# Kernel optimization log

Hardware: AMD Instinct MI355X
Metric: run time of the kernel (lower is better)

The kernel has to match this reference:

```python
import jax, jax.numpy as jnp
import numpy as np

H = 1024          # hidden_size
NH = 16           # num_heads
NKV = 16          # num_kv_heads
HD = 64           # head_dim
INTER = 2048      # intermediate_size
E = 8             # num_experts
TOPK = 2
EPS = 1e-6


def setup_inputs() -> dict:
    key = jax.random.key(0)
    ks = jax.random.split(key, 8)
    B, S = 4, 1024
    total_qkv = (NH + 2 * NKV) * HD
    return {
        "hidden_states": jax.random.normal(ks[0], (B, S, H), dtype=jnp.float32),
        "attention_mask": jnp.zeros((1, 1, S, S), dtype=jnp.float32),
        "input_layernorm": jnp.ones((H,), dtype=jnp.float32),
        "post_attention_layernorm": jnp.ones((H,), dtype=jnp.float32),
        "qkv_w": jax.random.normal(ks[1], (H, total_qkv), dtype=jnp.float32) * 0.02,
        "o_w": jax.random.normal(ks[2], (NH * HD, H), dtype=jnp.float32) * 0.02,
        "router_w": jax.random.normal(ks[3], (H, E), dtype=jnp.float32) * 0.02,
        "gate_up_proj": jax.random.normal(ks[4], (E, H, 2 * INTER), dtype=jnp.float32) * 0.02,
        "down_proj": jax.random.normal(ks[5], (E, INTER, H), dtype=jnp.float32) * 0.02,
    }


def _rmsnorm(x, w):
    var = jnp.mean(x * x, axis=-1, keepdims=True)
    return x * jax.lax.rsqrt(var + EPS) * w


def _attention_block(x, attention_mask, input_layernorm, qkv_w, o_w):
    B, S, _ = x.shape
    h = _rmsnorm(x, input_layernorm)
    qkv = h @ qkv_w  # [B,S,(NH+2*NKV)*HD]
    tq, tkv = NH * HD, NKV * HD
    q = qkv[..., :tq].reshape(B, S, NH, HD).transpose(0, 2, 1, 3)
    k = qkv[..., tq:tq + tkv].reshape(B, S, NKV, HD).transpose(0, 2, 1, 3)
    v = qkv[..., tq + tkv:].reshape(B, S, NKV, HD).transpose(0, 2, 1, 3)
    scores = jnp.einsum('bhqd,bhkd->bhqk', q, k) / np.sqrt(HD).astype(np.float32)
    scores = scores + attention_mask
    attn = jax.nn.softmax(scores, axis=-1)
    out = jnp.einsum('bhqk,bhkd->bhqd', attn, v)
    out = out.transpose(0, 2, 1, 3).reshape(B, S, NH * HD)
    return out @ o_w


def _moe_block(x, post_attention_layernorm, router_w, gate_up_proj, down_proj):
    B, S, _ = x.shape
    xf = x.reshape(-1, H)                      # [T,H]
    T = xf.shape[0]
    hf = _rmsnorm(xf, post_attention_layernorm)
    logits = hf @ router_w                     # [T,E]
    probs = jax.nn.softmax(logits, axis=-1)
    w, idx = jax.lax.top_k(probs, TOPK)        # [T,TOPK]
    w = w / jnp.sum(w, axis=-1, keepdims=True)
    # combine weights scattered into dense [T,E] (0 for unrouted experts)
    cw = jnp.zeros((T, E), dtype=hf.dtype).at[jnp.arange(T)[:, None], idx].add(w)
    out = jnp.zeros_like(hf)
    for e in range(E):  # fixed small expert loop, fully vectorized over tokens
        gu = hf @ gate_up_proj[e]              # [T,2*INTER]
        g, u = gu[:, :INTER], gu[:, INTER:]
        act = jax.nn.silu(g) * u
        out = out + cw[:, e:e + 1] * (act @ down_proj[e])
    return out.reshape(B, S, H)


def reference(hidden_states, attention_mask, input_layernorm, post_attention_layernorm,
              qkv_w, o_w, router_w, gate_up_proj, down_proj):
    x = hidden_states
    x = x + _attention_block(x, attention_mask, input_layernorm, qkv_w, o_w)
    x = x + _moe_block(x, post_attention_layernorm, router_w, gate_up_proj, down_proj)
    return x
```

## Files before the change

kernel.cpp:

```cpp
#include <hip/hip_runtime.h>
#include <cstdint>
#include <cmath>

#define T_TOK 4096
#define H_DIM 1024
#define QKV_N 3072
#define S_LEN 1024
#define INTER_DIM 2048
#define MAXROWS 9216

typedef unsigned short u16;
using f32x4 = __attribute__((ext_vector_type(4))) float;
using h16x8 = __attribute__((ext_vector_type(8))) _Float16;
using h16x4 = __attribute__((ext_vector_type(4))) _Float16;
using i32x4 = __attribute__((ext_vector_type(4))) int;
using u16x4 = __attribute__((ext_vector_type(4))) u16;
using u16x8 = __attribute__((ext_vector_type(8))) u16;

__device__ __forceinline__ float bf2f(u16 u){ return __uint_as_float(((uint32_t)u)<<16); }
__device__ __forceinline__ u16 f2bf(float f){
  uint32_t x = __float_as_uint(f);
  uint32_t r = x + 0x7FFFu + ((x>>16)&1u);
  return (u16)(r>>16);
}
__device__ __forceinline__ f32x4 mfma16(h16x8 a, h16x8 b, f32x4 c){
  return __builtin_amdgcn_mfma_f32_16x16x32_f16(a,b,c,0,0,0);
}
__device__ __forceinline__ float rsqrt_acc(float v){
  float r = rsqrtf(v);
  r = r*(1.5f - 0.5f*v*r*r);
  r = r*(1.5f - 0.5f*v*r*r);
  return r;
}
__device__ __forceinline__ float ldin(const void* p, size_t i, int is32){
  return is32 ? ((const float*)p)[i] : bf2f(((const u16*)p)[i]);
}
__device__ __forceinline__ int kslot_sw(int k, int noct){
  return (k&7) | (((k>>3) ^ (noct&3))<<3);
}
__device__ __forceinline__ void gll16(const void* g, void* l){
  __builtin_amdgcn_global_load_lds(
      (const __attribute__((address_space(1))) void*)g,
      (__attribute__((address_space(3))) void*)l, 16, 0, 0);
}

__global__ void k_detect(const uint32_t* __restrict__ x, int* __restrict__ dflag){
  uint32_t u = x[threadIdx.x];
  int e = (u>>23)&0xFF;
  int ok = (e>=103 && e<=150);
  unsigned long long m = __ballot(ok);
  if (threadIdx.x==0) *dflag = (__popcll(m) >= 48) ? 1 : 0;
}

__global__ __launch_bounds__(256) void k_trans2(const void* __restrict__ src,
    _Float16* __restrict__ dst, int R, int C, const int* __restrict__ df){
  const int is32 = *df;
  __shared__ _Float16 t[64][65];
  size_t bo = (size_t)blockIdx.z * R * C;
  int c0 = blockIdx.x<<6, r0 = blockIdx.y<<6;
  int ty = threadIdx.x>>3, tx = threadIdx.x&7;
  #pragma unroll
  for (int rr=0; rr<2; rr++){
    int r = rr*32 + ty;
    size_t gi = bo + (size_t)(r0+r)*C + c0 + tx*8;
    _Float16 v[8];
    if (is32){
      f32x4 a0 = *(const f32x4*)&((const float*)src)[gi];
      f32x4 a1 = *(const f32x4*)&((const float*)src)[gi+4];
      #pragma unroll
      for (int i=0;i<4;i++){ v[i]=(_Float16)a0[i]; v[4+i]=(_Float16)a1[i]; }
    } else {
      u16x8 a = *(const u16x8*)&((const u16*)src)[gi];
      #pragma unroll
      for (int i=0;i<8;i++) v[i]=(_Float16)bf2f(a[i]);
    }
    #pragma unroll
    for (int i=0;i<8;i++) t[r][tx*8+i] = v[i];
  }
  __syncthreads();
  #pragma unroll
  for (int rr=0; rr<2; rr++){
    int n = rr*32 + ty;
    h16x8 v;
    #pragma unroll
    for (int i=0;i<8;i++) v[i] = t[tx*8+i][n];
    *(h16x8*)&dst[bo + (size_t)(c0+n)*R + r0 + tx*8] = v;
  }
}

__global__ __launch_bounds__(256) void k_maskchk(const void* __restrict__ m, int* __restrict__ flag,
                                                 const int* __restrict__ df){
  const int is32 = *df;
  int i = (blockIdx.x*256 + threadIdx.x)*4;
  int nz = 0;
  if (is32){
    f32x4 v = *(const f32x4*)&((const float*)m)[i];
    nz = (v[0]!=0.f)||(v[1]!=0.f)||(v[2]!=0.f)||(v[3]!=0.f);
  } else {
    u16x4 v = *(const u16x4*)&((const u16*)m)[i];
    nz = ((v[0]|v[1]|v[2]|v[3]) & 0x7FFF) != 0;
  }
  if (nz) atomicOr(flag, 1);
}

__global__ __launch_bounds__(256) void k_rms1(const void* __restrict__ x, const void* __restrict__ w,
                                              float* __restrict__ h, const int* __restrict__ df){
  const int is32 = *df;
  int t = blockIdx.x, tid = threadIdx.x;
  size_t base = (size_t)t*H_DIM + tid*4;
  float f[4];
  #pragma unroll
  for (int m=0;m<4;m++) f[m] = ldin(x, base+m, is32);
  float ss = f[0]*f[0] + f[1]*f[1] + f[2]*f[2] + f[3]*f[3];
  #pragma unroll
  for (int off=32; off>0; off>>=1) ss += __shfl_down(ss, off, 64);
  __shared__ float red[4];
  if ((tid & 63) == 0) red[tid>>6] = ss;
  __syncthreads();
  float rstd = rsqrt_acc((red[0]+red[1]+red[2]+red[3]) * (1.0f/H_DIM) + 1e-6f);
  f32x4 o;
  #pragma unroll
  for (int m=0;m<4;m++) o[m] = f[m]*rstd*ldin(w, tid*4+m, is32);
  *(f32x4*)&h[base] = o;
}

template<int EPI>
__global__ __launch_bounds__(256) void k_gemm_splitA(const float* __restrict__ A,
    const _Float16* __restrict__ Bt, float* __restrict__ C, const void* __restrict__ res,
    int N, int K, const int* __restrict__ df){
  const int is32 = *df;
  __shared__ __align__(16) _Float16 Ahi[128*32];
  __shared__ __align__(16) _Float16 Alo[128*32];
  __shared__ __align__(16) _Float16 Bs[128*32];
  int tid = threadIdx.x, lane = tid&63, wvx = tid>>6;
  int wr = wvx>>1, wc = wvx&1, quad = lane>>4, lrow = lane&15;
  int m0 = blockIdx.y<<7, n0 = blockIdx.x<<7;
  f32x4 acc[4][4] = {};
  for (int k0=0; k0<K; k0+=32){
    #pragma unroll
    for (int it=0; it<4; it++){
      int ch = it*256 + tid;
      int r = ch>>3, g = ch&7;
      f32x4 v = *(const f32x4*)&A[(size_t)(m0+r)*K + k0 + g*4];
      h16x4 hi, lo;
      #pragma unroll
      for (int q2=0;q2<4;q2++){
        _Float16 hh = (_Float16)v[q2];
        hi[q2] = hh;
        lo[q2] = (_Float16)(v[q2] - (float)hh);
      }
      *(h16x4*)&Ahi[r*32 + g*4] = hi;
      *(h16x4*)&Alo[r*32 + g*4] = lo;
    }
    #pragma unroll
    for (int it=0; it<2; it++){
      int ch = it*256 + tid;
      gll16(&Bt[(size_t)(n0 + (ch>>2))*K + k0 + (ch&3)*8], &Bs[(size_t)(it*256 + wvx*64)*8]);
    }
    __syncthreads();
    h16x8 ah[4], al[4], bb[4];
    #pragma unroll
    for (int i=0;i<4;i++){
      ah[i] = *(const h16x8*)&Ahi[(wr*64 + i*16 + lrow)*32 + quad*8];
      al[i] = *(const h16x8*)&Alo[(wr*64 + i*16 + lrow)*32 + quad*8];
    }
    #pragma unroll
    for (int j=0;j<4;j++) bb[j] = *(const h16x8*)&Bs[(wc*64 + j*16 + lrow)*32 + quad*8];
    #pragma unroll
    for (int i=0;i<4;i++)
      #pragma unroll
      for (int j=0;j<4;j++){
        acc[i][j] = mfma16(ah[i], bb[j], acc[i][j]);
        acc[i][j] = mfma16(al[i], bb[j], acc[i][j]);
      }
    __syncthreads();
  }
  #pragma unroll
  for (int i=0;i<4;i++)
    #pragma unroll
    for (int j=0;j<4;j++){
      int col = n0 + wc*64 + j*16 + lrow;
      #pragma unroll
      for (int r=0;r<4;r++){
        int row = m0 + wr*64 + i*16 + quad*4 + r;
        size_t idx = (size_t)row*N + col;
        float v = acc[i][j][r];
        if (EPI==1) v += ldin(res, idx, is32);
        C[idx] = v;
      }
    }
}

__global__ __launch_bounds__(256) void k_attn(const float* __restrict__ qkv, const void* __restrict__ mask,
                                              const int* __restrict__ mflag, float* __restrict__ aout,
                                              const int* __restrict__ df){
  const int is32 = *df;
  __shared__ __align__(16) _Float16 Qhi[2*128*32], Qlo[2*128*32];
  __shared__ __align__(16) _Float16 Khi[2*32*32],  Klo[2*32*32];
  __shared__ __align__(16) _Float16 Vhi[64*32],    Vlo[64*32];
  __shared__ __align__(16) _Float16 Phi[128*32],   Plo[128*32];
  int qt = blockIdx.x, bh = blockIdx.y;
  int b = bh>>4, h = bh&15;
  int tid = threadIdx.x, lane = tid&63, wvx = tid>>6, quad = lane>>4, lrow = lane&15;
  size_t tok0 = (size_t)b*S_LEN;
  int q0 = qt<<7;
  #pragma unroll
  for (int it=0; it<8; it++){
    int idx = it*256 + tid;
    int r = idx>>4, g = idx&15;
    int d0 = g*4, p = g>>3;
    f32x4 v = *(const f32x4*)&qkv[(tok0 + q0 + r)*QKV_N + h*64 + d0];
    h16x4 hi, lo;
    #pragma unroll
    for (int m=0;m<4;m++){ _Float16 hh=(_Float16)v[m]; hi[m]=hh; lo[m]=(_Float16)(v[m]-(float)hh); }
    *(h16x4*)&Qhi[(p*128 + r)*32 + (d0&31)] = hi;
    *(h16x4*)&Qlo[(p*128 + r)*32 + (d0&31)] = lo;
  }
  int useMask = *mflag;
  float mrun[2][4], lrun[2][4];
  f32x4 oacc[2][4] = {};
  #pragma unroll
  for (int i=0;i<2;i++)
    #pragma unroll
    for (int r=0;r<4;r++){ mrun[i][r] = -INFINITY; lrun[i][r] = 0.f; }

  for (int kt=0; kt<32; kt++){
    int key0 = kt*32;
    __syncthreads();
    #pragma unroll
    for (int it=0; it<2; it++){
      int idx = it*256 + tid;
      int key = idx>>4, g = idx&15;
      int d0 = g*4, p = g>>3;
      f32x4 v = *(const f32x4*)&qkv[(tok0 + key0 + key)*QKV_N + 1024 + h*64 + d0];
      h16x4 hi, lo;
      #pragma unroll
      for (int m=0;m<4;m++){ _Float16 hh=(_Float16)v[m]; hi[m]=hh; lo[m]=(_Float16)(v[m]-(float)hh); }
      *(h16x4*)&Khi[(p*32 + key)*32 + (d0&31)] = hi;
      *(h16x4*)&Klo[(p*32 + key)*32 + (d0&31)] = lo;
    }
    #pragma unroll
    for (int it=0; it<2; it++){
      int idx = it*256 + tid;
      int key = idx & 31, dg = idx >> 5;
      int d0 = dg*4;
      f32x4 v = *(const f32x4*)&qkv[(tok0 + key0 + key)*QKV_N + 2048 + h*64 + d0];
      #pragma unroll
      for (int m=0;m<4;m++){
        _Float16 hh = (_Float16)v[m];
        Vhi[(d0+m)*32 + key] = hh;
        Vlo[(d0+m)*32 + key] = (_Float16)(v[m]-(float)hh);
      }
    }
    __syncthreads();
    f32x4 sacc[2][2] = {};
    #pragma unroll
    for (int p=0;p<2;p++){
      h16x8 qh[2], ql[2], kh[2], kl[2];
      #pragma unroll
      for (int i=0;i<2;i++){
        qh[i] = *(const h16x8*)&Qhi[(p*128 + wvx*32 + i*16 + lrow)*32 + quad*8];
        ql[i] = *(const h16x8*)&Qlo[(p*128 + wvx*32 + i*16 + lrow)*32 + quad*8];
      }
      #pragma unroll
      for (int j=0;j<2;j++){
        kh[j] = *(const h16x8*)&Khi[(p*32 + j*16 + lrow)*32 + quad*8];
        kl[j] = *(const h16x8*)&Klo[(p*32 + j*16 + lrow)*32 + quad*8];
      }
      #pragma unroll
      for (int i=0;i<2;i++)
        #pragma unroll
        for (int j=0;j<2;j++){
          sacc[i][j] = mfma16(qh[i], kh[j], sacc[i][j]);
          sacc[i][j] = mfma16(qh[i], kl[j], sacc[i][j]);
          sacc[i][j] = mfma16(ql[i], kh[j], sacc[i][j]);
        }
    }
    #pragma unroll
    for (int i=0;i<2;i++){
      #pragma unroll
      for (int r=0;r<4;r++){
        int qrow = q0 + wvx*32 + i*16 + quad*4 + r;
        #pragma unroll
        for (int j=0;j<2;j++){
          float s = sacc[i][j][r] * 0.125f;
          if (useMask) s += ldin(mask, (size_t)qrow*S_LEN + key0 + j*16 + lrow, is32);
          sacc[i][j][r] = s;
        }
        float mx = fmaxf(sacc[i][0][r], sacc[i][1][r]);
        #pragma unroll
        for (int mm=1; mm<=8; mm<<=1) mx = fmaxf(mx, __shfl_xor(mx, mm, 64));
        float mnew = fmaxf(mrun[i][r], mx);
        float alpha = __expf(mrun[i][r] - mnew);
        float ps = 0.f;
        #pragma unroll
        for (int j=0;j<2;j++){
          float p = __expf(sacc[i][j][r] - mnew);
          sacc[i][j][r] = p;
          ps += p;
        }
        #pragma unroll
        for (int mm=1; mm<=8; mm<<=1) ps += __shfl_xor(ps, mm, 64);
        lrun[i][r] = lrun[i][r]*alpha + ps;
        mrun[i][r] = mnew;
        #pragma unroll
        for (int j=0;j<4;j++) oacc[i][j][r] *= alpha;
        int prow = wvx*32 + i*16 + quad*4 + r;
        #pragma unroll
        for (int j=0;j<2;j++){
          int key = j*16 + lrow;
          float pv = sacc[i][j][r];
          _Float16 ph = (_Float16)pv;
          Phi[prow*32 + key] = ph;
          Plo[prow*32 + key] = (_Float16)(pv - (float)ph);
        }
      }
    }
    __syncthreads();
    {
      h16x8 pf[2], pl[2], vh[4], vl[4];
      #pragma unroll
      for (int i=0;i<2;i++){
        pf[i] = *(const h16x8*)&Phi[(wvx*32 + i*16 + lrow)*32 + quad*8];
        pl[i] = *(const h16x8*)&Plo[(wvx*32 + i*16 + lrow)*32 + quad*8];
      }
      #pragma unroll
      for (int j=0;j<4;j++){
        vh[j] = *(const h16x8*)&Vhi[(j*16 + lrow)*32 + quad*8];
        vl[j] = *(const h16x8*)&Vlo[(j*16 + lrow)*32 + quad*8];
      }
      #pragma unroll
      for (int i=0;i<2;i++)
        #pragma unroll
        for (int j=0;j<4;j++){
          oacc[i][j] = mfma16(pf[i], vh[j], oacc[i][j]);
          oacc[i][j] = mfma16(pf[i], vl[j], oacc[i][j]);
          oacc[i][j] = mfma16(pl[i], vh[j], oacc[i][j]);
        }
    }
  }
  #pragma unroll
  for (int i=0;i<2;i++)
    #pragma unroll
    for (int j=0;j<4;j++)
      #pragma unroll
      for (int r=0;r<4;r++){
        int row = q0 + wvx*32 + i*16 + quad*4 + r;
        int col = h*64 + j*16 + lrow;
        aout[(tok0 + row)*H_DIM + col] = oacc[i][j][r] / lrun[i][r];
      }
}

__global__ __launch_bounds__(256) void k_rms2_router(const float* __restrict__ x1, const void* __restrict__ w,
    const void* __restrict__ rw, _Float16* __restrict__ h2,
    int* __restrict__ tok_e, float* __restrict__ tok_w, int* __restrict__ counts,
    const int* __restrict__ df){
  const int is32 = *df;
  int t = blockIdx.x, tid = threadIdx.x;
  f32x4 v = *(const f32x4*)&x1[(size_t)t*H_DIM + tid*4];
  float ss = v[0]*v[0]+v[1]*v[1]+v[2]*v[2]+v[3]*v[3];
  #pragma unroll
  for (int off=32; off>0; off>>=1) ss += __shfl_down(ss, off, 64);
  __shared__ float red[4];
  __shared__ float lgs[32];
  if ((tid&63)==0) red[tid>>6] = ss;
  __syncthreads();
  float rstd = rsqrt_acc((red[0]+red[1]+red[2]+red[3])*(1.0f/H_DIM) + 1e-6f);
  float hv[4];
  h16x4 hst;
  #pragma unroll
  for (int m=0;m<4;m++){ hv[m] = v[m]*rstd*ldin(w, tid*4+m, is32); hst[m] = (_Float16)hv[m]; }
  *(h16x4*)&h2[(size_t)t*H_DIM + tid*4] = hst;
  float part[8] = {0,0,0,0,0,0,0,0};
  #pragma unroll
  for (int m=0;m<4;m++){
    size_t c = (size_t)(tid*4 + m)*8;
    #pragma unroll
    for (int e=0;e<8;e++) part[e] += hv[m]*ldin(rw, c+e, is32);
  }
  #pragma unroll
  for (int e=0;e<8;e++){
    #pragma unroll
    for (int off=32; off>0; off>>=1) part[e] += __shfl_down(part[e], off, 64);
  }
  if ((tid&63)==0){
    #pragma unroll
    for (int e=0;e<8;e++) lgs[(tid>>6)*8 + e] = part[e];
  }
  __syncthreads();
  if (tid==0){
    float lg[8];
    #pragma unroll
    for (int e=0;e<8;e++) lg[e] = lgs[e] + lgs[8+e] + lgs[16+e] + lgs[24+e];
    int e0 = 0;
    #pragma unroll
    for (int e=1;e<8;e++) if (lg[e] > lg[e0]) e0 = e;
    int e1 = (e0==0) ? 1 : 0;
    #pragma unroll
    for (int e=0;e<8;e++) if (e != e0 && lg[e] > lg[e1]) e1 = e;
    float d = expf(lg[e1] - lg[e0]);
    float w0 = 1.0f/(1.0f + d);
    float w1 = d * w0;
    tok_e[t*2] = e0; tok_e[t*2+1] = e1;
    tok_w[t*2] = w0; tok_w[t*2+1] = w1;
    atomicAdd(&counts[e0], 1);
    atomicAdd(&counts[e1], 1);
  }
}

__global__ void k_offsets(const int* __restrict__ counts, int* __restrict__ offs, int* __restrict__ fillpos){
  if (threadIdx.x == 0 && blockIdx.x == 0){
    int o = 0;
    for (int e=0;e<8;e++){
      offs[e] = o; fillpos[e] = o;
      o += (counts[e] + 127) & ~127;
    }
    offs[8] = o;
  }
}

__global__ __launch_bounds__(256) void k_fill(const int* __restrict__ tok_e, const float* __restrict__ tok_w,
    int* __restrict__ fillpos, int* __restrict__ list_ts, float* __restrict__ list_w){
  int t = blockIdx.x*256 + threadIdx.x;
  if (t >= T_TOK) return;
  #pragma unroll
  for (int s=0;s<2;s++){
    int e = tok_e[t*2+s];
    int p = atomicAdd(&fillpos[e], 1);
    list_ts[p] = t*2 + s;
    list_w[p] = tok_w[t*2+s];
  }
}


__global__ __launch_bounds__(256) void k_gemm_gu_t(const _Float16* __restrict__ h2,
    const _Float16* __restrict__ gwt, _Float16* __restrict__ act, const int* __restrict__ list_ts,
    const int* __restrict__ counts, const int* __restrict__ offs){
  int m0 = blockIdx.y<<7;
  if (m0 >= offs[8]) return;
  int e = 0;
  while (m0 >= offs[e+1]) e++;
  int base = offs[e], cnt = counts[e];
  if (m0 >= base + cnt) return;
  __shared__ __align__(16) _Float16 As[128*32], Bg[64*32], Bu[64*32];
  __shared__ int rowtok[128];
  int tid = threadIdx.x;
  if (tid < 128) rowtok[tid] = list_ts[min(m0 + tid, base + cnt - 1)] >> 1;
  __syncthreads();
  int lane = tid&63, wvx = tid>>6, wr = wvx>>1, wc = wvx&1, quad = lane>>4, lrow = lane&15;
  int n0 = blockIdx.x<<6;
  const _Float16* Bge = gwt + (size_t)e*4096*1024 + (size_t)n0*1024;
  const _Float16* Bue = gwt + (size_t)e*4096*1024 + (size_t)(2048+n0)*1024;
  const _Float16* arow0 = &h2[(size_t)rowtok[tid>>2]*H_DIM + (tid&3)*8];
  const _Float16* arow1 = &h2[(size_t)rowtok[(256+tid)>>2]*H_DIM + (tid&3)*8];
  int bR = tid>>2, bG = tid&3;
  f32x4 ag[4][2] = {}, au[4][2] = {};
  for (int k0=0; k0<1024; k0+=32){
    gll16(arow0 + k0, &As[(size_t)(wvx*64)*8]);
    gll16(arow1 + k0, &As[(size_t)(256 + wvx*64)*8]);
    gll16(&Bge[(size_t)bR*1024 + k0 + bG*8], &Bg[(size_t)(wvx*64)*8]);
    gll16(&Bue[(size_t)bR*1024 + k0 + bG*8], &Bu[(size_t)(wvx*64)*8]);
    __syncthreads();
    h16x8 a[4], bg[2], bu[2];
    #pragma unroll
    for (int i=0;i<4;i++) a[i] = *(const h16x8*)&As[(wr*64 + i*16 + lrow)*32 + quad*8];
    #pragma unroll
    for (int j=0;j<2;j++){
      bg[j] = *(const h16x8*)&Bg[(wc*32 + j*16 + lrow)*32 + quad*8];
      bu[j] = *(const h16x8*)&Bu[(wc*32 + j*16 + lrow)*32 + quad*8];
    }
    #pragma unroll
    for (int i=0;i<4;i++)
      #pragma unroll
      for (int j=0;j<2;j++){
        ag[i][j] = mfma16(a[i], bg[j], ag[i][j]);
        au[i][j] = mfma16(a[i], bu[j], au[i][j]);
      }
    __syncthreads();
  }
  #pragma unroll
  for (int i=0;i<4;i++)
    #pragma unroll
    for (int j=0;j<2;j++)
      #pragma unroll
      for (int r=0;r<4;r++){
        int row = m0 + wr*64 + i*16 + quad*4 + r;
        int col = n0 + wc*32 + j*16 + lrow;
        float g = ag[i][j][r], u = au[i][j][r];
        float sv = g / (1.0f + __expf(-g));
        act[(size_t)row*INTER_DIM + col] = (_Float16)(sv * u);
      }
}

__global__ __launch_bounds__(256) void k_gemm_down_t(const _Float16* __restrict__ act,
    const _Float16* __restrict__ dwt, _Float16* __restrict__ slotbuf, const int* __restrict__ list_ts,
    const float* __restrict__ list_w, const int* __restrict__ counts, const int* __restrict__ offs){
  int m0 = blockIdx.y<<7;
  if (m0 >= offs[8]) return;
  int e = 0;
  while (m0 >= offs[e+1]) e++;
  int base = offs[e], cnt = counts[e];
  if (m0 >= base + cnt) return;
  __shared__ __align__(16) _Float16 As[128*32], Bs[128*32];
  int tid = threadIdx.x, lane = tid&63, wvx = tid>>6;
  int wr = wvx>>1, wc = wvx&1, quad = lane>>4, lrow = lane&15;
  int n0 = blockIdx.x<<7;
  const _Float16* Be = dwt + (size_t)e*1024*2048 + (size_t)n0*2048;
  f32x4 acc[4][4] = {};
  for (int k0=0; k0<2048; k0+=32){
    #pragma unroll
    for (int it=0; it<2; it++){
      int c2 = it*256 + tid;
      int r = c2>>2, g = c2&3;
      gll16(&act[(size_t)(m0+r)*INTER_DIM + k0 + g*8], &As[(size_t)(it*256 + wvx*64)*8]);
      gll16(&Be[(size_t)r*2048 + k0 + g*8], &Bs[(size_t)(it*256 + wvx*64)*8]);
    }
    __syncthreads();
    h16x8 a[4], b[4];
    #pragma unroll
    for (int i=0;i<4;i++) a[i] = *(const h16x8*)&As[(wr*64 + i*16 + lrow)*32 + quad*8];
    #pragma unroll
    for (int j=0;j<4;j++) b[j] = *(const h16x8*)&Bs[(wc*64 + j*16 + lrow)*32 + quad*8];
    #pragma unroll
    for (int i=0;i<4;i++)
      #pragma unroll
      for (int j=0;j<4;j++)
        acc[i][j] = mfma16(a[i], b[j], acc[i][j]);
    __syncthreads();
  }
  #pragma unroll
  for (int i=0;i<4;i++)
    #pragma unroll
    for (int r=0;r<4;r++){
      int m = m0 + wr*64 + i*16 + quad*4 + r;
      if (m < base + cnt){
        int ts = list_ts[m];
        float wgt = list_w[m];
        #pragma unroll
        for (int j=0;j<4;j++){
          int col = n0 + wc*64 + j*16 + lrow;
          slotbuf[(size_t)ts*H_DIM + col] = (_Float16)(wgt * acc[i][j][r]);
        }
      }
    }
}


__global__ __launch_bounds__(256) void k_gemm_gu(const _Float16* __restrict__ h2, const void* __restrict__ guw,
    _Float16* __restrict__ act, const int* __restrict__ list_ts,
    const int* __restrict__ counts, const int* __restrict__ offs, const int* __restrict__ df){
  const int is32 = *df;
  int m0 = blockIdx.y<<7;
  if (m0 >= offs[8]) return;
  int e = 0;
  while (m0 >= offs[e+1]) e++;
  int base = offs[e], cnt = counts[e];
  if (m0 >= base + cnt) return;
  __shared__ __align__(16) _Float16 As[128*32], Bg[64*40], Bu[64*40];
  __shared__ int rowtok[128];
  int tid = threadIdx.x;
  if (tid < 128){
    int mc = min(m0 + tid, base + cnt - 1);
    rowtok[tid] = list_ts[mc] >> 1;
  }
  __syncthreads();
  int lane = tid&63, wvx = tid>>6, wr = wvx>>1, wc = wvx&1, quad = lane>>4, lrow = lane&15;
  int n0 = blockIdx.x<<6;
  size_t ebase = (size_t)e*H_DIM*4096;
  f32x4 ag[4][2] = {}, au[4][2] = {};
  for (int k0=0; k0<1024; k0+=32){
    #pragma unroll
    for (int it=0; it<2; it++){
      int ch = it*256 + tid;
      int r = ch>>2, c = ch&3;
      *(i32x4*)&As[ch*8] = *(const i32x4*)&h2[(size_t)rowtok[r]*H_DIM + k0 + c*8];
    }
    {
      int k = tid>>3, g = tid&7;
      size_t rowb = ebase + (size_t)(k0+k)*4096;
      int ks = kslot_sw(k, g);
      _Float16 tg[8], tu[8];
      if (is32){
        const float* gf = (const float*)guw;
        f32x4 a0 = *(const f32x4*)&gf[rowb + n0 + g*8];
        f32x4 a1 = *(const f32x4*)&gf[rowb + n0 + g*8 + 4];
        f32x4 b0 = *(const f32x4*)&gf[rowb + 2048 + n0 + g*8];
        f32x4 b1 = *(const f32x4*)&gf[rowb + 2048 + n0 + g*8 + 4];
        #pragma unroll
        for (int i=0;i<4;i++){ tg[i]=(_Float16)a0[i]; tg[4+i]=(_Float16)a1[i];
                               tu[i]=(_Float16)b0[i]; tu[4+i]=(_Float16)b1[i]; }
      } else {
        const u16* gb = (const u16*)guw;
        u16x4 a0 = *(const u16x4*)&gb[rowb + n0 + g*8];
        u16x4 a1 = *(const u16x4*)&gb[rowb + n0 + g*8 + 4];
        u16x4 b0 = *(const u16x4*)&gb[rowb + 2048 + n0 + g*8];
        u16x4 b1 = *(const u16x4*)&gb[rowb + 2048 + n0 + g*8 + 4];
        #pragma unroll
        for (int i=0;i<4;i++){ tg[i]=(_Float16)bf2f(a0[i]); tg[4+i]=(_Float16)bf2f(a1[i]);
                               tu[i]=(_Float16)bf2f(b0[i]); tu[4+i]=(_Float16)bf2f(b1[i]); }
      }
      #pragma unroll
      for (int i=0;i<8;i++){
        int n = g*8 + i;
        Bg[n*40 + ks] = tg[i];
        Bu[n*40 + ks] = tu[i];
      }
    }
    __syncthreads();
    h16x8 a[4], bg[2], bu[2];
    #pragma unroll
    for (int i=0;i<4;i++) a[i] = *(const h16x8*)&As[(wr*64 + i*16 + lrow)*32 + quad*8];
    #pragma unroll
    for (int j=0;j<2;j++){
      int n = wc*32 + j*16 + lrow;
      int oct = (quad ^ ((n>>3)&3))*8;
      bg[j] = *(const h16x8*)&Bg[n*40 + oct];
      bu[j] = *(const h16x8*)&Bu[n*40 + oct];
    }
    #pragma unroll
    for (int i=0;i<4;i++)
      #pragma unroll
      for (int j=0;j<2;j++){
        ag[i][j] = mfma16(a[i], bg[j], ag[i][j]);
        au[i][j] = mfma16(a[i], bu[j], au[i][j]);
      }
    __syncthreads();
  }
  #pragma unroll
  for (int i=0;i<4;i++)
    #pragma unroll
    for (int j=0;j<2;j++)
      #pragma unroll
      for (int r=0;r<4;r++){
        int row = m0 + wr*64 + i*16 + quad*4 + r;
        int col = n0 + wc*32 + j*16 + lrow;
        float g = ag[i][j][r], u = au[i][j][r];
        float sv = g / (1.0f + __expf(-g));
        act[(size_t)row*INTER_DIM + col] = (_Float16)(sv * u);
      }
}

__global__ __launch_bounds__(256) void k_gemm_down(const _Float16* __restrict__ act, const void* __restrict__ dw,
    _Float16* __restrict__ slotbuf, const int* __restrict__ list_ts, const float* __restrict__ list_w,
    const int* __restrict__ counts, const int* __restrict__ offs, const int* __restrict__ df){
  const int is32 = *df;
  int m0 = blockIdx.y<<7;
  if (m0 >= offs[8]) return;
  int e = 0;
  while (m0 >= offs[e+1]) e++;
  int base = offs[e], cnt = counts[e];
  if (m0 >= base + cnt) return;
  __shared__ __align__(16) _Float16 As[128*32], Bs[128*40];
  int tid = threadIdx.x, lane = tid&63, wvx = tid>>6;
  int wr = wvx>>1, wc = wvx&1, quad = lane>>4, lrow = lane&15;
  int n0 = blockIdx.x<<7;
  size_t ebase = (size_t)e*INTER_DIM*H_DIM;
  f32x4 acc[4][4] = {};
  for (int k0=0; k0<2048; k0+=32){
    #pragma unroll
    for (int it=0; it<2; it++){
      int ch = it*256 + tid;
      int r = ch>>2, c = ch&3;
      *(i32x4*)&As[ch*8] = *(const i32x4*)&act[(size_t)(m0+r)*INTER_DIM + k0 + c*8];
    }
    {
      int k = tid>>3, g = tid&7;
      size_t rowb = ebase + (size_t)(k0+k)*H_DIM;
      int ks = kslot_sw(k, g);
      #pragma unroll
      for (int p=0;p<2;p++){
        _Float16 tb[8];
        if (is32){
          const float* bf = (const float*)dw;
          f32x4 a0 = *(const f32x4*)&bf[rowb + n0 + p*64 + g*8];
          f32x4 a1 = *(const f32x4*)&bf[rowb + n0 + p*64 + g*8 + 4];
          #pragma unroll
          for (int i=0;i<4;i++){ tb[i]=(_Float16)a0[i]; tb[4+i]=(_Float16)a1[i]; }
        } else {
          const u16* bb = (const u16*)dw;
          u16x4 a0 = *(const u16x4*)&bb[rowb + n0 + p*64 + g*8];
          u16x4 a1 = *(const u16x4*)&bb[rowb + n0 + p*64 + g*8 + 4];
          #pragma unroll
          for (int i=0;i<4;i++){ tb[i]=(_Float16)bf2f(a0[i]); tb[4+i]=(_Float16)bf2f(a1[i]); }
        }
        #pragma unroll
        for (int i=0;i<8;i++){
          int n = p*64 + g*8 + i;
          Bs[n*40 + ks] = tb[i];
        }
      }
    }
    __syncthreads();
    h16x8 a[4], b[4];
    #pragma unroll
    for (int i=0;i<4;i++) a[i] = *(const h16x8*)&As[(wr*64 + i*16 + lrow)*32 + quad*8];
    #pragma unroll
    for (int j=0;j<4;j++){
      int n = wc*64 + j*16 + lrow;
      b[j] = *(const h16x8*)&Bs[n*40 + ((quad ^ ((n>>3)&3))*8)];
    }
    #pragma unroll
    for (int i=0;i<4;i++)
      #pragma unroll
      for (int j=0;j<4;j++)
        acc[i][j] = mfma16(a[i], b[j], acc[i][j]);
    __syncthreads();
  }
  #pragma unroll
  for (int i=0;i<4;i++)
    #pragma unroll
    for (int r=0;r<4;r++){
      int m = m0 + wr*64 + i*16 + quad*4 + r;
      if (m < base + cnt){
        int ts = list_ts[m];
        float wgt = list_w[m];
        #pragma unroll
        for (int j=0;j<4;j++){
          int col = n0 + wc*64 + j*16 + lrow;
          slotbuf[(size_t)ts*H_DIM + col] = (_Float16)(wgt * acc[i][j][r]);
        }
      }
    }
}

__global__ __launch_bounds__(256) void k_final(const float* __restrict__ x1, const _Float16* __restrict__ slot,
                                               void* __restrict__ outv, const int* __restrict__ df){
  const int is32 = *df;
  int i4 = (blockIdx.x*256 + threadIdx.x)*4;
  int t = i4 >> 10, c = i4 & 1023;
  f32x4 a = *(const f32x4*)&x1[i4];
  h16x4 s0 = *(const h16x4*)&slot[(size_t)(t*2)*H_DIM + c];
  h16x4 s1 = *(const h16x4*)&slot[(size_t)(t*2+1)*H_DIM + c];
  if (is32){
    f32x4 o;
    #pragma unroll
    for (int m=0;m<4;m++) o[m] = a[m] + (float)s0[m] + (float)s1[m];
    *(f32x4*)&((float*)outv)[i4] = o;
  } else {
    u16x4 o;
    #pragma unroll
    for (int m=0;m<4;m++) o[m] = f2bf(a[m] + (float)s0[m] + (float)s1[m]);
    *(u16x4*)&((u16*)outv)[i4] = o;
  }
}

extern "C" void kernel_launch(void* const* d_in, const int* in_sizes, int n_in,
                              void* d_out, int out_size, void* d_ws, size_t ws_size,
                              hipStream_t stream){
  (void)in_sizes; (void)n_in; (void)out_size;
  const void* x    = d_in[0];
  const void* mask = d_in[1];
  const void* ln1  = d_in[2];
  const void* ln2  = d_in[3];
  const void* qkvw = d_in[4];
  const void* ow   = d_in[5];
  const void* rw   = d_in[6];
  const void* guw  = d_in[7];
  const void* dww  = d_in[8];

  char* ws = (char*)d_ws;
  size_t off = 0;
  auto alloc = [&](size_t b)->void*{ void* p = ws + off; off = (off + b + 255) & ~(size_t)255; return p; };
  int* meta            = (int*)alloc(32*sizeof(int));
  _Float16* qkv_wt     = (_Float16*)alloc((size_t)3072*1024*2);
  _Float16* o_wt       = (_Float16*)alloc((size_t)1024*1024*2);
  float* hbuf          = (float*)alloc((size_t)4096*1024*4);
  float* qkvbuf        = (float*)alloc((size_t)4096*3072*4);
  float* x1            = (float*)alloc((size_t)4096*1024*4);
  int* list_ts         = (int*)alloc(MAXROWS*4);
  float* list_w        = (float*)alloc(MAXROWS*4);
  int* tok_e           = (int*)alloc((size_t)4096*2*4);
  float* tok_w         = (float*)alloc((size_t)4096*2*4);
  size_t base_end = off;
  _Float16* gu_wt      = (_Float16*)alloc((size_t)8*4096*1024*2);
  _Float16* down_wt    = (_Float16*)alloc((size_t)8*1024*2048*2);
  const int big = (ws_size >= off) ? 1 : 0;
  (void)base_end;

  int* counts = meta;
  int* offs   = meta + 8;
  int* fillpos= meta + 17;
  int* flag   = meta + 25;
  int* dflag  = meta + 26;
  _Float16* h2      = (_Float16*)qkvbuf;
  _Float16* act     = (_Float16*)((char*)qkvbuf + (size_t)4096*1024*2);
  _Float16* slotbuf = (_Float16*)hbuf;

  hipMemsetAsync(meta, 0, 32*sizeof(int), stream);
  k_detect<<<dim3(1), dim3(64), 0, stream>>>((const uint32_t*)x, dflag);
  k_trans2<<<dim3(48, 16, 1), 256, 0, stream>>>(qkvw, qkv_wt, 1024, 3072, dflag);
  k_trans2<<<dim3(16, 16, 1), 256, 0, stream>>>(ow, o_wt, 1024, 1024, dflag);
  if (big){
    k_trans2<<<dim3(64, 16, 8), 256, 0, stream>>>(guw, gu_wt, 1024, 4096, dflag);
    k_trans2<<<dim3(16, 32, 8), 256, 0, stream>>>(dww, down_wt, 2048, 1024, dflag);
  }
  k_maskchk<<<dim3(1024), 256, 0, stream>>>(mask, flag, dflag);
  k_rms1<<<dim3(4096), 256, 0, stream>>>(x, ln1, hbuf, dflag);
  k_gemm_splitA<0><<<dim3(24, 32), 256, 0, stream>>>(hbuf, qkv_wt, qkvbuf, nullptr, 3072, 1024, dflag);
  k_attn<<<dim3(8, 64), 256, 0, stream>>>(qkvbuf, mask, flag, hbuf, dflag);
  k_gemm_splitA<1><<<dim3(8, 32), 256, 0, stream>>>(hbuf, o_wt, x1, x, 1024, 1024, dflag);
  k_rms2_router<<<dim3(4096), 256, 0, stream>>>(x1, ln2, rw, h2, tok_e, tok_w, counts, dflag);
  k_offsets<<<dim3(1), dim3(64), 0, stream>>>(counts, offs, fillpos);
  k_fill<<<dim3(16), 256, 0, stream>>>(tok_e, tok_w, fillpos, list_ts, list_w);
  if (big){
    k_gemm_gu_t<<<dim3(32, 72), 256, 0, stream>>>(h2, gu_wt, act, list_ts, counts, offs);
    k_gemm_down_t<<<dim3(8, 72), 256, 0, stream>>>(act, down_wt, slotbuf, list_ts, list_w, counts, offs);
  } else {
    k_gemm_gu<<<dim3(32, 72), 256, 0, stream>>>(h2, guw, act, list_ts, counts, offs, dflag);
    k_gemm_down<<<dim3(8, 72), 256, 0, stream>>>(act, dww, slotbuf, list_ts, list_w, counts, offs, dflag);
  }
  k_final<<<dim3(4096), 256, 0, stream>>>(x1, slotbuf, d_out, dflag);
}
```

Baseline: 920.0 us.

## Store activations as pre-split fp16 hi/lo pairs and pre-transpose V for attention

RMSNorm, the QKV GEMM and attention now emit fp16 hi/lo split pairs instead of fp32, so the downstream GEMMs and attention load their operands directly into LDS with async global-to-LDS copies and skip the per-tile split and convert work. A new kernel pre-transposes V into a per-head dim-major layout so attention can load V tiles without scattered LDS stores. Attention also keeps Q fragments in registers, shares one LDS pool, raises wave priority around the MFMA blocks and sets launch bounds to 3 blocks. This costs an extra kernel launch and repurposes buffers (x1 holds the transposed V), which adds aliasing risk.

```diff
diff --git a/kernel.cpp b/kernel.cpp
--- a/kernel.cpp
+++ b/kernel.cpp
@@ -104,7 +104,8 @@
 }
 
 __global__ __launch_bounds__(256) void k_rms1(const void* __restrict__ x, const void* __restrict__ w,
-                                              float* __restrict__ h, const int* __restrict__ df){
+                                              _Float16* __restrict__ hhi, _Float16* __restrict__ hlo,
+                                              const int* __restrict__ df){
   const int is32 = *df;
   int t = blockIdx.x, tid = threadIdx.x;
   size_t base = (size_t)t*H_DIM + tid*4;
@@ -118,51 +119,51 @@
   if ((tid & 63) == 0) red[tid>>6] = ss;
   __syncthreads();
   float rstd = rsqrt_acc((red[0]+red[1]+red[2]+red[3]) * (1.0f/H_DIM) + 1e-6f);
-  f32x4 o;
-  #pragma unroll
-  for (int m=0;m<4;m++) o[m] = f[m]*rstd*ldin(w, tid*4+m, is32);
-  *(f32x4*)&h[base] = o;
+  h16x4 oh, ol;
+  #pragma unroll
+  for (int m=0;m<4;m++){
+    float v = f[m]*rstd*ldin(w, tid*4+m, is32);
+    _Float16 hh = (_Float16)v;
+    oh[m] = hh;
+    ol[m] = (_Float16)(v - (float)hh);
+  }
+  *(h16x4*)&hhi[base] = oh;
+  *(h16x4*)&hlo[base] = ol;
 }
 
 template<int EPI>
-__global__ __launch_bounds__(256) void k_gemm_splitA(const float* __restrict__ A,
-    const _Float16* __restrict__ Bt, float* __restrict__ C, const void* __restrict__ res,
-    int N, int K, const int* __restrict__ df){
-  const int is32 = *df;
-  __shared__ __align__(16) _Float16 Ahi[128*32];
-  __shared__ __align__(16) _Float16 Alo[128*32];
+__global__ __launch_bounds__(256) void k_gemm_hl(const _Float16* __restrict__ Ah,
+    const _Float16* __restrict__ Al, const _Float16* __restrict__ Bt,
+    float* __restrict__ C, _Float16* __restrict__ Chi, _Float16* __restrict__ Clo,
+    const void* __restrict__ res, int N, int K, const int* __restrict__ df){
+  const int is32 = (EPI==1) ? *df : 0;
+  __shared__ __align__(16) _Float16 AhS[128*32];
+  __shared__ __align__(16) _Float16 AlS[128*32];
   __shared__ __align__(16) _Float16 Bs[128*32];
   int tid = threadIdx.x, lane = tid&63, wvx = tid>>6;
   int wr = wvx>>1, wc = wvx&1, quad = lane>>4, lrow = lane&15;
   int m0 = blockIdx.y<<7, n0 = blockIdx.x<<7;
+  int ar = tid>>2, acg = (tid&3)*8;
+  const _Float16* a0h = &Ah[(size_t)(m0+ar)*K + acg];
+  const _Float16* a1h = &Ah[(size_t)(m0+64+ar)*K + acg];
+  const _Float16* a0l = &Al[(size_t)(m0+ar)*K + acg];
+  const _Float16* a1l = &Al[(size_t)(m0+64+ar)*K + acg];
+  const _Float16* b0  = &Bt[(size_t)(n0+ar)*K + acg];
+  const _Float16* b1  = &Bt[(size_t)(n0+64+ar)*K + acg];
   f32x4 acc[4][4] = {};
   for (int k0=0; k0<K; k0+=32){
-    #pragma unroll
-    for (int it=0; it<4; it++){
-      int ch = it*256 + tid;
-      int r = ch>>3, g = ch&7;
-      f32x4 v = *(const f32x4*)&A[(size_t)(m0+r)*K + k0 + g*4];
-      h16x4 hi, lo;
-      #pragma unroll
-      for (int q2=0;q2<4;q2++){
-        _Float16 hh = (_Float16)v[q2];
-        hi[q2] = hh;
-        lo[q2] = (_Float16)(v[q2] - (float)hh);
-      }
-      *(h16x4*)&Ahi[r*32 + g*4] = hi;
-      *(h16x4*)&Alo[r*32 + g*4] = lo;
-    }
-    #pragma unroll
-    for (int it=0; it<2; it++){
-      int ch = it*256 + tid;
-      gll16(&Bt[(size_t)(n0 + (ch>>2))*K + k0 + (ch&3)*8], &Bs[(size_t)(it*256 + wvx*64)*8]);
-    }
+    gll16(a0h + k0, &AhS[wvx*512]);
+    gll16(a1h + k0, &AhS[2048 + wvx*512]);
+    gll16(a0l + k0, &AlS[wvx*512]);
+    gll16(a1l + k0, &AlS[2048 + wvx*512]);
+    gll16(b0  + k0, &Bs[wvx*512]);
+    gll16(b1  + k0, &Bs[2048 + wvx*512]);
     __syncthreads();
     h16x8 ah[4], al[4], bb[4];
     #pragma unroll
     for (int i=0;i<4;i++){
-      ah[i] = *(const h16x8*)&Ahi[(wr*64 + i*16 + lrow)*32 + quad*8];
-      al[i] = *(const h16x8*)&Alo[(wr*64 + i*16 + lrow)*32 + quad*8];
+      ah[i] = *(const h16x8*)&AhS[(wr*64 + i*16 + lrow)*32 + quad*8];
+      al[i] = *(const h16x8*)&AlS[(wr*64 + i*16 + lrow)*32 + quad*8];
     }
     #pragma unroll
     for (int j=0;j<4;j++) bb[j] = *(const h16x8*)&Bs[(wc*64 + j*16 + lrow)*32 + quad*8];
@@ -185,37 +186,87 @@
         int row = m0 + wr*64 + i*16 + quad*4 + r;
         size_t idx = (size_t)row*N + col;
         float v = acc[i][j][r];
-        if (EPI==1) v += ldin(res, idx, is32);
-        C[idx] = v;
-      }
-    }
-}
-
-__global__ __launch_bounds__(256) void k_attn(const float* __restrict__ qkv, const void* __restrict__ mask,
-                                              const int* __restrict__ mflag, float* __restrict__ aout,
-                                              const int* __restrict__ df){
+        if (EPI==1){
+          v += ldin(res, idx, is32);
+          C[idx] = v;
+        } else {
+          _Float16 hh = (_Float16)v;
+          Chi[idx] = hh;
+          Clo[idx] = (_Float16)(v - (float)hh);
+        }
+      }
+    }
+}
+
+__global__ __launch_bounds__(256) void k_vt(const _Float16* __restrict__ qh,
+    const _Float16* __restrict__ ql, _Float16* __restrict__ vth, _Float16* __restrict__ vtl){
+  __shared__ _Float16 th[64][72];
+  __shared__ _Float16 tl[64][72];
+  int bh = blockIdx.y;
+  int b = bh>>4, h = bh&15;
+  int key0 = blockIdx.x<<6;
+  size_t tok0 = (size_t)b*S_LEN;
+  int ty = threadIdx.x>>3, tx = threadIdx.x&7;
+  #pragma unroll
+  for (int rr=0; rr<2; rr++){
+    int r = rr*32 + ty;
+    size_t gi = (tok0 + key0 + r)*(size_t)QKV_N + 2048 + h*64 + tx*8;
+    h16x8 vh_ = *(const h16x8*)&qh[gi];
+    h16x8 vl_ = *(const h16x8*)&ql[gi];
+    #pragma unroll
+    for (int i=0;i<8;i++){ th[r][tx*8+i] = vh_[i]; tl[r][tx*8+i] = vl_[i]; }
+  }
+  __syncthreads();
+  size_t dbase = (size_t)bh*64*1024;
+  #pragma unroll
+  for (int rr=0; rr<2; rr++){
+    int d = rr*32 + ty;
+    h16x8 oh, ol;
+    #pragma unroll
+    for (int i=0;i<8;i++){ oh[i] = th[tx*8+i][d]; ol[i] = tl[tx*8+i][d]; }
+    *(h16x8*)&vth[dbase + (size_t)d*1024 + key0 + tx*8] = oh;
+    *(h16x8*)&vtl[dbase + (size_t)d*1024 + key0 + tx*8] = ol;
+  }
+}
+
+__global__ __launch_bounds__(256, 3) void k_attn(const _Float16* __restrict__ qkvh,
+    const _Float16* __restrict__ qkvl, const _Float16* __restrict__ vth_g,
+    const _Float16* __restrict__ vtl_g, const void* __restrict__ mask,
+    const int* __restrict__ mflag, _Float16* __restrict__ ohi, _Float16* __restrict__ olo,
+    const int* __restrict__ df){
   const int is32 = *df;
-  __shared__ __align__(16) _Float16 Qhi[2*128*32], Qlo[2*128*32];
-  __shared__ __align__(16) _Float16 Khi[2*32*32],  Klo[2*32*32];
-  __shared__ __align__(16) _Float16 Vhi[64*32],    Vlo[64*32];
-  __shared__ __align__(16) _Float16 Phi[128*32],   Plo[128*32];
+  __shared__ __align__(16) _Float16 pool[16384];
   int qt = blockIdx.x, bh = blockIdx.y;
   int b = bh>>4, h = bh&15;
   int tid = threadIdx.x, lane = tid&63, wvx = tid>>6, quad = lane>>4, lrow = lane&15;
   size_t tok0 = (size_t)b*S_LEN;
   int q0 = qt<<7;
-  #pragma unroll
-  for (int it=0; it<8; it++){
-    int idx = it*256 + tid;
-    int r = idx>>4, g = idx&15;
-    int d0 = g*4, p = g>>3;
-    f32x4 v = *(const f32x4*)&qkv[(tok0 + q0 + r)*QKV_N + h*64 + d0];
-    h16x4 hi, lo;
-    #pragma unroll
-    for (int m=0;m<4;m++){ _Float16 hh=(_Float16)v[m]; hi[m]=hh; lo[m]=(_Float16)(v[m]-(float)hh); }
-    *(h16x4*)&Qhi[(p*128 + r)*32 + (d0&31)] = hi;
-    *(h16x4*)&Qlo[(p*128 + r)*32 + (d0&31)] = lo;
-  }
+  {
+    int r = tid>>2, cg = (tid&3)*8;
+    #pragma unroll
+    for (int p=0;p<2;p++)
+      #pragma unroll
+      for (int g=0;g<2;g++){
+        size_t src = (tok0 + q0 + g*64 + r)*(size_t)QKV_N + h*64 + p*32 + cg;
+        gll16(&qkvh[src], &pool[p*4096 + g*2048 + wvx*512]);
+        gll16(&qkvl[src], &pool[8192 + p*4096 + g*2048 + wvx*512]);
+      }
+  }
+  __syncthreads();
+  h16x8 qfh[2][2], qfl[2][2];
+  #pragma unroll
+  for (int p=0;p<2;p++)
+    #pragma unroll
+    for (int i=0;i<2;i++){
+      qfh[p][i] = *(const h16x8*)&pool[(p*128 + wvx*32 + i*16 + lrow)*32 + quad*8];
+      qfl[p][i] = *(const h16x8*)&pool[8192 + (p*128 + wvx*32 + i*16 + lrow)*32 + quad*8];
+    }
+  _Float16* Khi = pool;
+  _Float16* Klo = pool + 2048;
+  _Float16* Vth = pool + 4096;
+  _Float16* Vtl = pool + 6144;
+  _Float16* Phi = pool + 8192;
+  _Float16* Plo = pool + 12288;
   int useMask = *mflag;
   float mrun[2][4], lrun[2][4];
   f32x4 oacc[2][4] = {};
@@ -223,45 +274,27 @@
   for (int i=0;i<2;i++)
     #pragma unroll
     for (int r=0;r<4;r++){ mrun[i][r] = -INFINITY; lrun[i][r] = 0.f; }
+  size_t vbase = (size_t)bh*64*1024;
+  int kr = (tid>>2)&31, kp = tid>>7, kcg = (tid&3)*8;
+  int vd = tid>>2;
 
   for (int kt=0; kt<32; kt++){
     int key0 = kt*32;
     __syncthreads();
-    #pragma unroll
-    for (int it=0; it<2; it++){
-      int idx = it*256 + tid;
-      int key = idx>>4, g = idx&15;
-      int d0 = g*4, p = g>>3;
-      f32x4 v = *(const f32x4*)&qkv[(tok0 + key0 + key)*QKV_N + 1024 + h*64 + d0];
-      h16x4 hi, lo;
-      #pragma unroll
-      for (int m=0;m<4;m++){ _Float16 hh=(_Float16)v[m]; hi[m]=hh; lo[m]=(_Float16)(v[m]-(float)hh); }
-      *(h16x4*)&Khi[(p*32 + key)*32 + (d0&31)] = hi;
-      *(h16x4*)&Klo[(p*32 + key)*32 + (d0&31)] = lo;
-    }
-    #pragma unroll
-    for (int it=0; it<2; it++){
-      int idx = it*256 + tid;
-      int key = idx & 31, dg = idx >> 5;
-      int d0 = dg*4;
-      f32x4 v = *(const f32x4*)&qkv[(tok0 + key0 + key)*QKV_N + 2048 + h*64 + d0];
-      #pragma unroll
-      for (int m=0;m<4;m++){
-        _Float16 hh = (_Float16)v[m];
-        Vhi[(d0+m)*32 + key] = hh;
-        Vlo[(d0+m)*32 + key] = (_Float16)(v[m]-(float)hh);
-      }
+    {
+      size_t ks = (tok0 + key0 + kr)*(size_t)QKV_N + 1024 + h*64 + kp*32 + kcg;
+      gll16(&qkvh[ks], &Khi[wvx*512]);
+      gll16(&qkvl[ks], &Klo[wvx*512]);
+      size_t vs = vbase + (size_t)vd*1024 + key0 + (tid&3)*8;
+      gll16(&vth_g[vs], &Vth[wvx*512]);
+      gll16(&vtl_g[vs], &Vtl[wvx*512]);
     }
     __syncthreads();
     f32x4 sacc[2][2] = {};
+    __builtin_amdgcn_s_setprio(1);
     #pragma unroll
     for (int p=0;p<2;p++){
-      h16x8 qh[2], ql[2], kh[2], kl[2];
-      #pragma unroll
-      for (int i=0;i<2;i++){
-        qh[i] = *(const h16x8*)&Qhi[(p*128 + wvx*32 + i*16 + lrow)*32 + quad*8];
-        ql[i] = *(const h16x8*)&Qlo[(p*128 + wvx*32 + i*16 + lrow)*32 + quad*8];
-      }
+      h16x8 kh[2], kl[2];
       #pragma unroll
       for (int j=0;j<2;j++){
         kh[j] = *(const h16x8*)&Khi[(p*32 + j*16 + lrow)*32 + quad*8];
@@ -271,11 +304,12 @@
       for (int i=0;i<2;i++)
         #pragma unroll
         for (int j=0;j<2;j++){
-          sacc[i][j] = mfma16(qh[i], kh[j], sacc[i][j]);
-          sacc[i][j] = mfma16(qh[i], kl[j], sacc[i][j]);
-          sacc[i][j] = mfma16(ql[i], kh[j], sacc[i][j]);
-        }
-    }
+          sacc[i][j] = mfma16(qfh[p][i], kh[j], sacc[i][j]);
+          sacc[i][j] = mfma16(qfh[p][i], kl[j], sacc[i][j]);
+          sacc[i][j] = mfma16(qfl[p][i], kh[j], sacc[i][j]);
+        }
+    }
+    __builtin_amdgcn_s_setprio(0);
     #pragma unroll
     for (int i=0;i<2;i++){
       #pragma unroll
@@ -326,9 +360,10 @@
       }
       #pragma unroll
       for (int j=0;j<4;j++){
-        vh[j] = *(const h16x8*)&Vhi[(j*16 + lrow)*32 + quad*8];
-        vl[j] = *(const h16x8*)&Vlo[(j*16 + lrow)*32 + quad*8];
-      }
+        vh[j] = *(const h16x8*)&Vth[(j*16 + lrow)*32 + quad*8];
+        vl[j] = *(const h16x8*)&Vtl[(j*16 + lrow)*32 + quad*8];
+      }
+      __builtin_amdgcn_s_setprio(1);
       #pragma unroll
       for (int i=0;i<2;i++)
         #pragma unroll
@@ -337,6 +372,7 @@
           oacc[i][j] = mfma16(pf[i], vl[j], oacc[i][j]);
           oacc[i][j] = mfma16(pl[i], vh[j], oacc[i][j]);
         }
+      __builtin_amdgcn_s_setprio(0);
     }
   }
   #pragma unroll
@@ -347,7 +383,11 @@
       for (int r=0;r<4;r++){
         int row = q0 + wvx*32 + i*16 + quad*4 + r;
         int col = h*64 + j*16 + lrow;
-        aout[(tok0 + row)*H_DIM + col] = oacc[i][j][r] / lrun[i][r];
+        size_t idx = (tok0 + row)*H_DIM + col;
+        float v = oacc[i][j][r] / lrun[i][r];
+        _Float16 hh = (_Float16)v;
+        ohi[idx] = hh;
+        olo[idx] = (_Float16)(v - (float)hh);
       }
 }
 
@@ -764,8 +804,8 @@
   int* meta            = (int*)alloc(32*sizeof(int));
   _Float16* qkv_wt     = (_Float16*)alloc((size_t)3072*1024*2);
   _Float16* o_wt       = (_Float16*)alloc((size_t)1024*1024*2);
-  float* hbuf          = (float*)alloc((size_t)4096*1024*4);
-  float* qkvbuf        = (float*)alloc((size_t)4096*3072*4);
+  _Float16* hpair      = (_Float16*)alloc((size_t)2*4096*1024*2);
+  _Float16* qkvpair    = (_Float16*)alloc((size_t)2*4096*3072*2);
   float* x1            = (float*)alloc((size_t)4096*1024*4);
   int* list_ts         = (int*)alloc(MAXROWS*4);
   float* list_w        = (float*)alloc(MAXROWS*4);
@@ -782,9 +822,18 @@
   int* fillpos= meta + 17;
   int* flag   = meta + 25;
   int* dflag  = meta + 26;
-  _Float16* h2      = (_Float16*)qkvbuf;
-  _Float16* act     = (_Float16*)((char*)qkvbuf + (size_t)4096*1024*2);
-  _Float16* slotbuf = (_Float16*)hbuf;
+
+  _Float16* h_hi   = hpair;
+  _Float16* h_lo   = hpair + (size_t)4096*1024;
+  _Float16* qkv_hi = qkvpair;
+  _Float16* qkv_lo = qkvpair + (size_t)4096*3072;
+  _Float16* vth    = (_Float16*)x1;
+  _Float16* vtl    = vth + (size_t)64*64*1024;
+  _Float16* ahi    = hpair;
+  _Float16* alo    = hpair + (size_t)4096*1024;
+  _Float16* h2     = qkvpair;
+  _Float16* act    = qkvpair + (size_t)4096*1024;
+  _Float16* slotbuf= hpair;
 
   hipMemsetAsync(meta, 0, 32*sizeof(int), stream);
   k_detect<<<dim3(1), dim3(64), 0, stream>>>((const uint32_t*)x, dflag);
@@ -795,10 +844,13 @@
     k_trans2<<<dim3(16, 32, 8), 256, 0, stream>>>(dww, down_wt, 2048, 1024, dflag);
   }
   k_maskchk<<<dim3(1024), 256, 0, stream>>>(mask, flag, dflag);
-  k_rms1<<<dim3(4096), 256, 0, stream>>>(x, ln1, hbuf, dflag);
-  k_gemm_splitA<0><<<dim3(24, 32), 256, 0, stream>>>(hbuf, qkv_wt, qkvbuf, nullptr, 3072, 1024, dflag);
-  k_attn<<<dim3(8, 64), 256, 0, stream>>>(qkvbuf, mask, flag, hbuf, dflag);
-  k_gemm_splitA<1><<<dim3(8, 32), 256, 0, stream>>>(hbuf, o_wt, x1, x, 1024, 1024, dflag);
+  k_rms1<<<dim3(4096), 256, 0, stream>>>(x, ln1, h_hi, h_lo, dflag);
+  k_gemm_hl<0><<<dim3(24, 32), 256, 0, stream>>>(h_hi, h_lo, qkv_wt, nullptr, qkv_hi, qkv_lo,
+                                                 nullptr, 3072, 1024, dflag);
+  k_vt<<<dim3(16, 64), 256, 0, stream>>>(qkv_hi, qkv_lo, vth, vtl);
+  k_attn<<<dim3(8, 64), 256, 0, stream>>>(qkv_hi, qkv_lo, vth, vtl, mask, flag, ahi, alo, dflag);
+  k_gemm_hl<1><<<dim3(8, 32), 256, 0, stream>>>(ahi, alo, o_wt, x1, nullptr, nullptr,
+                                                x, 1024, 1024, dflag);
   k_rms2_router<<<dim3(4096), 256, 0, stream>>>(x1, ln2, rw, h2, tok_e, tok_w, counts, dflag);
   k_offsets<<<dim3(1), dim3(64), 0, stream>>>(counts, offs, fillpos);
   k_fill<<<dim3(16), 256, 0, stream>>>(tok_e, tok_w, fillpos, list_ts, list_w);
```

Result: faster. 884.2 us (-3.9%).
